# Performance work log

Hardware: AMD Instinct MI355X
Metric: run time of the kernel (lower is better)

## Reference

```python
import jax, jax.numpy as jnp
import numpy as np

N, D, C, P = 4096, 512, 100, 64
EPS_COS = 1e-8   # torch cosine_similarity norm clamp
EPS_INV = 1e-5   # module's 1/(d + 1e-5)


def setup_inputs() -> dict:
    key = jax.random.key(0)
    k1, k2, k3, k4 = jax.random.split(key, 4)
    feats = jax.random.normal(k1, (N, D), dtype=jnp.float32)
    protos = jax.random.normal(k2, (C, P, D), dtype=jnp.float32)
    cls_ids = jax.random.randint(k3, (N,), 0, C)
    proto_labels = jax.random.randint(k4, (C, P), 0, 1000)
    return {"feats": feats, "protos": protos, "cls_ids": cls_ids,
            "proto_labels": proto_labels}


def reference(feats, protos, cls_ids, proto_labels):
    # Gather each box's class-conditional prototype set: [N, P, D]
    p = protos[cls_ids]
    pl = proto_labels[cls_ids]                       # [N, P]

    # cosine distance: 1 - f.p / (max(|f|,eps) * max(|p|,eps))
    dot = jnp.einsum('nd,npd->np', feats, p)         # [N, P]
    fnorm = jnp.maximum(jnp.linalg.norm(feats, axis=-1, keepdims=True), EPS_COS)
    pnorm = jnp.maximum(jnp.linalg.norm(p, axis=-1), EPS_COS)
    d_cos = 1.0 - dot / (fnorm * pnorm)

    diff = feats[:, None, :] - p                     # [N, P, D]
    d_l1 = jnp.mean(jnp.abs(diff), axis=-1)          # F.l1_loss (mean)
    d_l2 = jnp.mean(diff * diff, axis=-1)            # F.mse_loss (mean)

    dists = jnp.stack([d_cos, d_l1, d_l2], axis=1)   # [N, 3, P]
    probs = jax.nn.softmax(1.0 / (dists + EPS_INV), axis=-1).mean(axis=1)  # [N, P]

    idx = jnp.argmax(probs, axis=-1)                 # [N]
    labels = jnp.take_along_axis(pl, idx[:, None], axis=1)[:, 0]
    return labels, probs
```

## Files before the change

### kernel.cpp

```cpp
#include <hip/hip_runtime.h>

#define D 512
#define D4 (D / 4)
#define P 64
#define WPB 4
#define BPB 8
#define MAXC 256
#define EPS_COS 1e-8f
#define EPS_INV 1e-5f

__device__ __forceinline__ float wave_sum(float v) {
#pragma unroll
    for (int m = 32; m >= 1; m >>= 1) v += __shfl_xor(v, m, 64);
    return v;
}

__global__ __launch_bounds__(256) void prep_kernel(
    const float* __restrict__ protos, float* __restrict__ pp, int rows,
    const int* __restrict__ cls_ids, int* __restrict__ bcount,
    int* __restrict__ blockClass, int* __restrict__ slots,
    int N, int C, int normBlocks)
{
    const int bid = blockIdx.x;

    if (bid < normBlocks) {
        const int lane = threadIdx.x & 63;
        const int wave = threadIdx.x >> 6;
        const int r = bid * WPB + wave;
        if (r >= rows) return;
        const float* row = protos + (size_t)r * D;
        const float4 a = *(const float4*)(row + lane * 4);
        const float4 b = *(const float4*)(row + 256 + lane * 4);
        float s = a.x*a.x + a.y*a.y + a.z*a.z + a.w*a.w
                + b.x*b.x + b.y*b.y + b.z*b.z + b.w*b.w;
        s = wave_sum(s);
        if (lane == 0) pp[r] = s;
        return;
    }

    __shared__ int cnt[MAXC], blkb[MAXC], fil[MAXC];
    __shared__ int sv[256];
    const int tid = threadIdx.x;
    for (int c = tid; c < MAXC; c += 256) { cnt[c] = 0; fil[c] = 0; }
    __syncthreads();
    for (int n = tid; n < N; n += 256) atomicAdd(&cnt[cls_ids[n]], 1);
    __syncthreads();
    int v = 0;
    if (tid < C) v = (cnt[tid] + BPB - 1) / BPB;
    sv[tid] = v;
    __syncthreads();
#pragma unroll
    for (int off = 1; off < 256; off <<= 1) {
        const int t = (tid >= off) ? sv[tid - off] : 0;
        __syncthreads();
        sv[tid] += t;
        __syncthreads();
    }
    const int B = sv[255];
    if (tid < C) blkb[tid] = sv[tid] - v;
    if (tid == 0) bcount[0] = B;
    __syncthreads();
    if (tid < C) {
        const int nb = (cnt[tid] + BPB - 1) / BPB;
        const int b0 = blkb[tid];
        for (int k = 0; k < nb; ++k) blockClass[b0 + k] = tid;
    }
    for (int i = tid; i < B * BPB; i += 256) slots[i] = -1;
    __syncthreads();
    for (int n = tid; n < N; n += 256) {
        const int c = cls_ids[n];
        const int r = atomicAdd(&fil[c], 1);
        slots[(blkb[c] + (r >> 3)) * BPB + (r & 7)] = n;
    }
}

__device__ __forceinline__ void box_epilogue(
    float r_dot, float r_l1, float ff, float s_pp, int myp,
    float& prob_o, int& bidx_o)
{
    const float fnorm = fmaxf(sqrtf(ff),   EPS_COS);
    const float pnorm = fmaxf(sqrtf(s_pp), EPS_COS);
    const float d_cos = 1.0f - r_dot / (fnorm * pnorm);
    const float d_l1  = r_l1 * (1.0f / (float)D);
    const float d_l2  = (ff - 2.0f * r_dot + s_pp) * (1.0f / (float)D);

    float s[3];
    s[0] = 1.0f / (d_cos + EPS_INV);
    s[1] = 1.0f / (d_l1  + EPS_INV);
    s[2] = 1.0f / (d_l2  + EPS_INV);

    float prob = 0.f;
#pragma unroll
    for (int i = 0; i < 3; ++i) {
        float m = s[i];
#pragma unroll
        for (int w = 32; w >= 1; w >>= 1) m = fmaxf(m, __shfl_xor(m, w, 64));
        const float e = expf(s[i] - m);
        const float denom = wave_sum(e);
        prob += e / denom;
    }
    prob *= (1.0f / 3.0f);

    float best = prob;
    int   bidx = myp;
#pragma unroll
    for (int w = 32; w >= 1; w >>= 1) {
        const float ov = __shfl_xor(best, w, 64);
        const int   oi = __shfl_xor(bidx, w, 64);
        if (ov > best || (ov == best && oi < bidx)) { best = ov; bidx = oi; }
    }
    prob_o = prob;
    bidx_o = bidx;
}

__global__ __launch_bounds__(WPB * 64) void proto_probs_kernel(
    const float* __restrict__ feats,
    const float* __restrict__ protos,
    const int*   __restrict__ proto_labels,
    const float* __restrict__ ppbuf,
    const int*   __restrict__ bcount,
    const int*   __restrict__ blockClass,
    const int*   __restrict__ slots,
    float* __restrict__ out,
    int N)
{
    const int tid  = threadIdx.x;
    const int lane = tid & 63;
    const int w    = tid >> 6;

    const int nbk = gridDim.x;
    const int q   = nbk >> 3, r = nbk & 7;
    const int xcd = blockIdx.x & 7, bix = blockIdx.x >> 3;
    const int b   = (xcd < r ? xcd * (q + 1) : r * (q + 1) + (xcd - r) * q) + bix;

    if (b >= bcount[0]) return;

    const int cls = __builtin_amdgcn_readfirstlane(blockClass[b]);
    const int s0  = __builtin_amdgcn_readfirstlane(slots[b * BPB]);
    const int k0  = __builtin_amdgcn_readfirstlane(slots[b * BPB + 2 * w]);
    const int k1  = __builtin_amdgcn_readfirstlane(slots[b * BPB + 2 * w + 1]);
    const int n0  = (k0 >= 0) ? k0 : s0;
    const int n1  = (k1 >= 0) ? k1 : s0;

    __shared__ float4 fLds[BPB * D4];
    __shared__ float4 pbuf[2 * 8 * P];

    const float4* feats4 = (const float4*)feats;
    const float*  prC    = protos + (size_t)cls * (P * D);

#pragma unroll
    for (int u = 0; u < 4; ++u) {
        const int i  = tid + 256 * u;
        const int bx = i >> 7;
        int nb = slots[b * BPB + bx];
        if (nb < 0) nb = s0;
        fLds[i] = feats4[(size_t)nb * D4 + (i & 127)];
    }

    const int jj  = tid & 7;
    const int pp0 = tid >> 3;
    {
        const float4 r0 = *(const float4*)(prC + (size_t)pp0 * D + jj * 4);
        const float4 r1 = *(const float4*)(prC + (size_t)(pp0 + 32) * D + jj * 4);
        pbuf[jj * 64 + pp0]      = r0;
        pbuf[jj * 64 + pp0 + 32] = r1;
    }
    __syncthreads();

    float ffA, ffB;
    {
        const float4 a0 = fLds[(2 * w) * D4 + lane];
        const float4 a1 = fLds[(2 * w) * D4 + 64 + lane];
        ffA = wave_sum(a0.x*a0.x + a0.y*a0.y + a0.z*a0.z + a0.w*a0.w
                     + a1.x*a1.x + a1.y*a1.y + a1.z*a1.z + a1.w*a1.w);
        const float4 c0 = fLds[(2 * w + 1) * D4 + lane];
        const float4 c1 = fLds[(2 * w + 1) * D4 + 64 + lane];
        ffB = wave_sum(c0.x*c0.x + c0.y*c0.y + c0.z*c0.z + c0.w*c0.w
                     + c1.x*c1.x + c1.y*c1.y + c1.z*c1.z + c1.w*c1.w);
    }

    float dotA = 0.f, l1A = 0.f, dotB = 0.f, l1B = 0.f;

#pragma unroll 1
    for (int c = 0; c < 16; ++c) {
        const int cur = c & 1;
        float4 s0r, s1r;
        if (c < 15) {
            s0r = *(const float4*)(prC + (size_t)pp0 * D + (c + 1) * 32 + jj * 4);
            s1r = *(const float4*)(prC + (size_t)(pp0 + 32) * D + (c + 1) * 32 + jj * 4);
        }
#pragma unroll
        for (int j = 0; j < 8; ++j) {
            const float4 qv = pbuf[cur * 512 + j * 64 + lane];
            const float4 av = fLds[(2 * w) * D4 + c * 8 + j];
            const float4 bv = fLds[(2 * w + 1) * D4 + c * 8 + j];
            float t;
            dotA += av.x*qv.x; t = av.x - qv.x; l1A += fabsf(t);
            dotA += av.y*qv.y; t = av.y - qv.y; l1A += fabsf(t);
            dotA += av.z*qv.z; t = av.z - qv.z; l1A += fabsf(t);
            dotA += av.w*qv.w; t = av.w - qv.w; l1A += fabsf(t);
            dotB += bv.x*qv.x; t = bv.x - qv.x; l1B += fabsf(t);
            dotB += bv.y*qv.y; t = bv.y - qv.y; l1B += fabsf(t);
            dotB += bv.z*qv.z; t = bv.z - qv.z; l1B += fabsf(t);
            dotB += bv.w*qv.w; t = bv.w - qv.w; l1B += fabsf(t);
        }
        if (c < 15) {
            pbuf[(cur ^ 1) * 512 + jj * 64 + pp0]      = s0r;
            pbuf[(cur ^ 1) * 512 + jj * 64 + pp0 + 32] = s1r;
        }
        __syncthreads();
    }

    const float s_pp = ppbuf[cls * P + lane];

    float probA; int bidxA;
    box_epilogue(dotA, l1A, ffA, s_pp, lane, probA, bidxA);
    if (k0 >= 0) {
        out[(size_t)N + (size_t)n0 * P + lane] = probA;
        if (lane == 0) out[n0] = (float)proto_labels[cls * P + bidxA];
    }
    if (k1 >= 0) {
        float probB; int bidxB;
        box_epilogue(dotB, l1B, ffB, s_pp, lane, probB, bidxB);
        out[(size_t)N + (size_t)n1 * P + lane] = probB;
        if (lane == 0) out[n1] = (float)proto_labels[cls * P + bidxB];
    }
}

extern "C" void kernel_launch(void* const* d_in, const int* in_sizes, int n_in,
                              void* d_out, int out_size, void* d_ws, size_t ws_size,
                              hipStream_t stream) {
    const float* feats        = (const float*)d_in[0];
    const float* protos       = (const float*)d_in[1];
    const int*   cls_ids      = (const int*)d_in[2];
    const int*   proto_labels = (const int*)d_in[3];
    float* out = (float*)d_out;

    const int N    = in_sizes[2];
    const int rows = in_sizes[1] / D;
    const int C    = rows / P;
    const int Bmax = (N + BPB - 1) / BPB + C;

    float* pp         = (float*)d_ws;
    int*   bcount     = (int*)(pp + rows);
    int*   blockClass = bcount + 1;
    int*   slots      = blockClass + Bmax;

    const int normBlocks = (rows + WPB - 1) / WPB;

    prep_kernel<<<normBlocks + 1, 256, 0, stream>>>(
        protos, pp, rows, cls_ids, bcount, blockClass, slots, N, C, normBlocks);
    proto_probs_kernel<<<Bmax, WPB * 64, 0, stream>>>(
        feats, protos, proto_labels, pp, bcount, blockClass, slots, out, N);
}
```

Baseline: 112.4 us.

## Fuse prep and compute into one kernel with per-block class bucketing

Drops the separate prep kernel. Each of C*8 blocks scans cls_ids on its own, builds its class's box list in shared memory with a prefix sum, and loops over its share of 8-box groups. Prototype squared norms are computed on the fly during the first group instead of in a separate pass. Features are now read straight from global memory instead of being staged in LDS. This removes one launch and the workspace round trip, but every block rescans all of cls_ids, and blocks can end up with uneven numbers of groups. The boxIds buffer holds only 512 entries, which caps the boxes per class and slice.

```diff
diff --git a/kernel.cpp b/kernel.cpp
--- a/kernel.cpp
+++ b/kernel.cpp
@@ -1,11 +1,10 @@
 #include <hip/hip_runtime.h>
 
 #define D 512
-#define D4 (D / 4)
+#define D4 128
 #define P 64
-#define WPB 4
-#define BPB 8
-#define MAXC 256
+#define NCHUNK 16
+#define SPB 8
 #define EPS_COS 1e-8f
 #define EPS_INV 1e-5f
 
@@ -15,63 +14,8 @@
     return v;
 }
 
-__global__ __launch_bounds__(256) void prep_kernel(
-    const float* __restrict__ protos, float* __restrict__ pp, int rows,
-    const int* __restrict__ cls_ids, int* __restrict__ bcount,
-    int* __restrict__ blockClass, int* __restrict__ slots,
-    int N, int C, int normBlocks)
-{
-    const int bid = blockIdx.x;
-
-    if (bid < normBlocks) {
-        const int lane = threadIdx.x & 63;
-        const int wave = threadIdx.x >> 6;
-        const int r = bid * WPB + wave;
-        if (r >= rows) return;
-        const float* row = protos + (size_t)r * D;
-        const float4 a = *(const float4*)(row + lane * 4);
-        const float4 b = *(const float4*)(row + 256 + lane * 4);
-        float s = a.x*a.x + a.y*a.y + a.z*a.z + a.w*a.w
-                + b.x*b.x + b.y*b.y + b.z*b.z + b.w*b.w;
-        s = wave_sum(s);
-        if (lane == 0) pp[r] = s;
-        return;
-    }
-
-    __shared__ int cnt[MAXC], blkb[MAXC], fil[MAXC];
-    __shared__ int sv[256];
-    const int tid = threadIdx.x;
-    for (int c = tid; c < MAXC; c += 256) { cnt[c] = 0; fil[c] = 0; }
-    __syncthreads();
-    for (int n = tid; n < N; n += 256) atomicAdd(&cnt[cls_ids[n]], 1);
-    __syncthreads();
-    int v = 0;
-    if (tid < C) v = (cnt[tid] + BPB - 1) / BPB;
-    sv[tid] = v;
-    __syncthreads();
-#pragma unroll
-    for (int off = 1; off < 256; off <<= 1) {
-        const int t = (tid >= off) ? sv[tid - off] : 0;
-        __syncthreads();
-        sv[tid] += t;
-        __syncthreads();
-    }
-    const int B = sv[255];
-    if (tid < C) blkb[tid] = sv[tid] - v;
-    if (tid == 0) bcount[0] = B;
-    __syncthreads();
-    if (tid < C) {
-        const int nb = (cnt[tid] + BPB - 1) / BPB;
-        const int b0 = blkb[tid];
-        for (int k = 0; k < nb; ++k) blockClass[b0 + k] = tid;
-    }
-    for (int i = tid; i < B * BPB; i += 256) slots[i] = -1;
-    __syncthreads();
-    for (int n = tid; n < N; n += 256) {
-        const int c = cls_ids[n];
-        const int r = atomicAdd(&fil[c], 1);
-        slots[(blkb[c] + (r >> 3)) * BPB + (r & 7)] = n;
-    }
+__device__ __forceinline__ float dot4(const float4 a, const float4 b) {
+    return a.x*b.x + a.y*b.y + a.z*b.z + a.w*b.w;
 }
 
 __device__ __forceinline__ void box_epilogue(
@@ -113,16 +57,13 @@
     bidx_o = bidx;
 }
 
-__global__ __launch_bounds__(WPB * 64) void proto_probs_kernel(
+__global__ __launch_bounds__(256) void fused_kernel(
     const float* __restrict__ feats,
     const float* __restrict__ protos,
+    const int*   __restrict__ cls_ids,
     const int*   __restrict__ proto_labels,
-    const float* __restrict__ ppbuf,
-    const int*   __restrict__ bcount,
-    const int*   __restrict__ blockClass,
-    const int*   __restrict__ slots,
     float* __restrict__ out,
-    int N)
+    int N, int C)
 {
     const int tid  = threadIdx.x;
     const int lane = tid & 63;
@@ -131,99 +72,156 @@
     const int nbk = gridDim.x;
     const int q   = nbk >> 3, r = nbk & 7;
     const int xcd = blockIdx.x & 7, bix = blockIdx.x >> 3;
-    const int b   = (xcd < r ? xcd * (q + 1) : r * (q + 1) + (xcd - r) * q) + bix;
-
-    if (b >= bcount[0]) return;
-
-    const int cls = __builtin_amdgcn_readfirstlane(blockClass[b]);
-    const int s0  = __builtin_amdgcn_readfirstlane(slots[b * BPB]);
-    const int k0  = __builtin_amdgcn_readfirstlane(slots[b * BPB + 2 * w]);
-    const int k1  = __builtin_amdgcn_readfirstlane(slots[b * BPB + 2 * w + 1]);
-    const int n0  = (k0 >= 0) ? k0 : s0;
-    const int n1  = (k1 >= 0) ? k1 : s0;
-
-    __shared__ float4 fLds[BPB * D4];
+    const int id  = (xcd < r ? xcd * (q + 1) : r * (q + 1) + (xcd - r) * q) + bix;
+    const int cls = id >> 3;
+    const int s   = id & 7;
+    if (cls >= C) return;
+
     __shared__ float4 pbuf[2 * 8 * P];
-
+    __shared__ int    sc[256];
+    __shared__ int    boxIds[512];
+    __shared__ float  ppLds[P];
+
+    unsigned mask = 0;
+    const int base = tid * 16;
+    {
+#pragma unroll
+        for (int k = 0; k < 16; k += 4) {
+            if (base + k + 3 < N) {
+                const int4 v = *(const int4*)(cls_ids + base + k);
+                if (v.x == cls) mask |= 1u << (k + 0);
+                if (v.y == cls) mask |= 1u << (k + 1);
+                if (v.z == cls) mask |= 1u << (k + 2);
+                if (v.w == cls) mask |= 1u << (k + 3);
+            } else {
+                for (int kk = k; kk < k + 4; ++kk)
+                    if (base + kk < N && cls_ids[base + kk] == cls)
+                        mask |= 1u << kk;
+            }
+        }
+    }
+    const int cnt = __popc(mask);
+    sc[tid] = cnt;
+    boxIds[tid] = -1;
+    boxIds[tid + 256] = -1;
+    __syncthreads();
+#pragma unroll
+    for (int off = 1; off < 256; off <<= 1) {
+        const int t = (tid >= off) ? sc[tid - off] : 0;
+        __syncthreads();
+        sc[tid] += t;
+        __syncthreads();
+    }
+    const int myBase = sc[tid] - cnt;
+    const int total  = sc[255];
+    {
+        int rk = myBase;
+        unsigned m2 = mask;
+        while (m2) {
+            const int k = __ffs(m2) - 1; m2 &= m2 - 1;
+            if (((rk >> 3) & 7) == s)
+                boxIds[((rk >> 6) << 3) | (rk & 7)] = base + k;
+            ++rk;
+        }
+    }
+    __syncthreads();
+
+    const int nb_total = (total + 7) >> 3;
+    const int nLoc = (nb_total > s) ? (((nb_total - 1 - s) >> 3) + 1) : 0;
+    if (nLoc == 0) return;
+
+    const float*  prC    = protos + (size_t)cls * (P * D);
     const float4* feats4 = (const float4*)feats;
-    const float*  prC    = protos + (size_t)cls * (P * D);
-
-#pragma unroll
-    for (int u = 0; u < 4; ++u) {
-        const int i  = tid + 256 * u;
-        const int bx = i >> 7;
-        int nb = slots[b * BPB + bx];
-        if (nb < 0) nb = s0;
-        fLds[i] = feats4[(size_t)nb * D4 + (i & 127)];
-    }
-
     const int jj  = tid & 7;
     const int pp0 = tid >> 3;
-    {
-        const float4 r0 = *(const float4*)(prC + (size_t)pp0 * D + jj * 4);
-        const float4 r1 = *(const float4*)(prC + (size_t)(pp0 + 32) * D + jj * 4);
-        pbuf[jj * 64 + pp0]      = r0;
-        pbuf[jj * 64 + pp0 + 32] = r1;
-    }
-    __syncthreads();
-
-    float ffA, ffB;
-    {
-        const float4 a0 = fLds[(2 * w) * D4 + lane];
-        const float4 a1 = fLds[(2 * w) * D4 + 64 + lane];
-        ffA = wave_sum(a0.x*a0.x + a0.y*a0.y + a0.z*a0.z + a0.w*a0.w
-                     + a1.x*a1.x + a1.y*a1.y + a1.z*a1.z + a1.w*a1.w);
-        const float4 c0 = fLds[(2 * w + 1) * D4 + lane];
-        const float4 c1 = fLds[(2 * w + 1) * D4 + 64 + lane];
-        ffB = wave_sum(c0.x*c0.x + c0.y*c0.y + c0.z*c0.z + c0.w*c0.w
-                     + c1.x*c1.x + c1.y*c1.y + c1.z*c1.z + c1.w*c1.w);
-    }
-
-    float dotA = 0.f, l1A = 0.f, dotB = 0.f, l1B = 0.f;
+
+    float qq0 = 0.f, qq1 = 0.f;
+
+    for (int L = 0; L < nLoc; ++L) {
+        const int sb    = L * 8;
+        const int first = __builtin_amdgcn_readfirstlane(boxIds[sb]);
+        const int k0    = __builtin_amdgcn_readfirstlane(boxIds[sb + 2 * w]);
+        const int k1    = __builtin_amdgcn_readfirstlane(boxIds[sb + 2 * w + 1]);
+        const int n0 = (k0 >= 0) ? k0 : first;
+        const int n1 = (k1 >= 0) ? k1 : first;
+
+        const float4* f0 = feats4 + (size_t)n0 * D4;
+        const float4* f1 = feats4 + (size_t)n1 * D4;
+
+        {
+            const float4 r0 = *(const float4*)(prC + (size_t)pp0 * D + jj * 4);
+            const float4 r1 = *(const float4*)(prC + (size_t)(pp0 + 32) * D + jj * 4);
+            if (L == 0) { qq0 += dot4(r0, r0); qq1 += dot4(r1, r1); }
+            pbuf[jj * 64 + pp0]      = r0;
+            pbuf[jj * 64 + pp0 + 32] = r1;
+        }
+
+        float ffA, ffB;
+        {
+            const float4 a0 = f0[lane], a1 = f0[64 + lane];
+            ffA = wave_sum(dot4(a0, a0) + dot4(a1, a1));
+            const float4 c0 = f1[lane], c1 = f1[64 + lane];
+            ffB = wave_sum(dot4(c0, c0) + dot4(c1, c1));
+        }
+        __syncthreads();
+
+        float dotA = 0.f, l1A = 0.f, dotB = 0.f, l1B = 0.f;
 
 #pragma unroll 1
-    for (int c = 0; c < 16; ++c) {
-        const int cur = c & 1;
-        float4 s0r, s1r;
-        if (c < 15) {
-            s0r = *(const float4*)(prC + (size_t)pp0 * D + (c + 1) * 32 + jj * 4);
-            s1r = *(const float4*)(prC + (size_t)(pp0 + 32) * D + (c + 1) * 32 + jj * 4);
-        }
-#pragma unroll
-        for (int j = 0; j < 8; ++j) {
-            const float4 qv = pbuf[cur * 512 + j * 64 + lane];
-            const float4 av = fLds[(2 * w) * D4 + c * 8 + j];
-            const float4 bv = fLds[(2 * w + 1) * D4 + c * 8 + j];
-            float t;
-            dotA += av.x*qv.x; t = av.x - qv.x; l1A += fabsf(t);
-            dotA += av.y*qv.y; t = av.y - qv.y; l1A += fabsf(t);
-            dotA += av.z*qv.z; t = av.z - qv.z; l1A += fabsf(t);
-            dotA += av.w*qv.w; t = av.w - qv.w; l1A += fabsf(t);
-            dotB += bv.x*qv.x; t = bv.x - qv.x; l1B += fabsf(t);
-            dotB += bv.y*qv.y; t = bv.y - qv.y; l1B += fabsf(t);
-            dotB += bv.z*qv.z; t = bv.z - qv.z; l1B += fabsf(t);
-            dotB += bv.w*qv.w; t = bv.w - qv.w; l1B += fabsf(t);
-        }
-        if (c < 15) {
-            pbuf[(cur ^ 1) * 512 + jj * 64 + pp0]      = s0r;
-            pbuf[(cur ^ 1) * 512 + jj * 64 + pp0 + 32] = s1r;
-        }
-        __syncthreads();
-    }
-
-    const float s_pp = ppbuf[cls * P + lane];
-
-    float probA; int bidxA;
-    box_epilogue(dotA, l1A, ffA, s_pp, lane, probA, bidxA);
-    if (k0 >= 0) {
-        out[(size_t)N + (size_t)n0 * P + lane] = probA;
-        if (lane == 0) out[n0] = (float)proto_labels[cls * P + bidxA];
-    }
-    if (k1 >= 0) {
-        float probB; int bidxB;
-        box_epilogue(dotB, l1B, ffB, s_pp, lane, probB, bidxB);
-        out[(size_t)N + (size_t)n1 * P + lane] = probB;
-        if (lane == 0) out[n1] = (float)proto_labels[cls * P + bidxB];
+        for (int c = 0; c < NCHUNK; ++c) {
+            const int cur = c & 1;
+            float4 s0r, s1r;
+            if (c < NCHUNK - 1) {
+                s0r = *(const float4*)(prC + (size_t)pp0 * D + (c + 1) * 32 + jj * 4);
+                s1r = *(const float4*)(prC + (size_t)(pp0 + 32) * D + (c + 1) * 32 + jj * 4);
+            }
+#pragma unroll
+            for (int j = 0; j < 8; ++j) {
+                const float4 qv = pbuf[cur * 512 + j * 64 + lane];
+                const float4 av = f0[c * 8 + j];
+                const float4 bv = f1[c * 8 + j];
+                float t;
+                dotA += av.x*qv.x; t = av.x - qv.x; l1A += fabsf(t);
+                dotA += av.y*qv.y; t = av.y - qv.y; l1A += fabsf(t);
+                dotA += av.z*qv.z; t = av.z - qv.z; l1A += fabsf(t);
+                dotA += av.w*qv.w; t = av.w - qv.w; l1A += fabsf(t);
+                dotB += bv.x*qv.x; t = bv.x - qv.x; l1B += fabsf(t);
+                dotB += bv.y*qv.y; t = bv.y - qv.y; l1B += fabsf(t);
+                dotB += bv.z*qv.z; t = bv.z - qv.z; l1B += fabsf(t);
+                dotB += bv.w*qv.w; t = bv.w - qv.w; l1B += fabsf(t);
+            }
+            if (c < NCHUNK - 1) {
+                if (L == 0) { qq0 += dot4(s0r, s0r); qq1 += dot4(s1r, s1r); }
+                pbuf[(cur ^ 1) * 512 + jj * 64 + pp0]      = s0r;
+                pbuf[(cur ^ 1) * 512 + jj * 64 + pp0 + 32] = s1r;
+            }
+            __syncthreads();
+        }
+
+        if (L == 0) {
+#pragma unroll
+            for (int m = 1; m <= 4; m <<= 1) {
+                qq0 += __shfl_xor(qq0, m, 64);
+                qq1 += __shfl_xor(qq1, m, 64);
+            }
+            if ((lane & 7) == 0) { ppLds[pp0] = qq0; ppLds[pp0 + 32] = qq1; }
+            __syncthreads();
+        }
+
+        const float s_pp = ppLds[lane];
+
+        float probA; int bidxA;
+        box_epilogue(dotA, l1A, ffA, s_pp, lane, probA, bidxA);
+        if (k0 >= 0) {
+            out[(size_t)N + (size_t)n0 * P + lane] = probA;
+            if (lane == 0) out[n0] = (float)proto_labels[cls * P + bidxA];
+        }
+        if (k1 >= 0) {
+            float probB; int bidxB;
+            box_epilogue(dotB, l1B, ffB, s_pp, lane, probB, bidxB);
+            out[(size_t)N + (size_t)n1 * P + lane] = probB;
+            if (lane == 0) out[n1] = (float)proto_labels[cls * P + bidxB];
+        }
     }
 }
 
@@ -236,20 +234,9 @@
     const int*   proto_labels = (const int*)d_in[3];
     float* out = (float*)d_out;
 
-    const int N    = in_sizes[2];
-    const int rows = in_sizes[1] / D;
-    const int C    = rows / P;
-    const int Bmax = (N + BPB - 1) / BPB + C;
-
-    float* pp         = (float*)d_ws;
-    int*   bcount     = (int*)(pp + rows);
-    int*   blockClass = bcount + 1;
-    int*   slots      = blockClass + Bmax;
-
-    const int normBlocks = (rows + WPB - 1) / WPB;
-
-    prep_kernel<<<normBlocks + 1, 256, 0, stream>>>(
-        protos, pp, rows, cls_ids, bcount, blockClass, slots, N, C, normBlocks);
-    proto_probs_kernel<<<Bmax, WPB * 64, 0, stream>>>(
-        feats, protos, proto_labels, pp, bcount, blockClass, slots, out, N);
-}
+    const int N = in_sizes[2];
+    const int C = in_sizes[1] / (D * P);
+
+    fused_kernel<<<C * SPB, 256, 0, stream>>>(
+        feats, protos, cls_ids, proto_labels, out, N, C);
+}
```

After: 111.1 us. About the same (-1.1%).
